# Kernel optimization log

Measured on AMD Instinct MI355X. Metric: run time of the kernel, lower is better.

Reference implementation:

```python
import jax, jax.numpy as jnp
import numpy as np

B, T_ENC, T_DEC = 1024, 96, 16
P_Q, CFG, H = 235, 32, 256
D_IN = P_Q + 5 + 10 + 3 + 3  # 256, matches input_size in __init__


def _lstm_step(x, h, c, Wih, Whh, bih, bhh):
    # torch.nn.LSTMCell: gate order i, f, g, o
    g = x @ Wih.T + bih + h @ Whh.T + bhh
    i, f, gg, o = jnp.split(g, 4, axis=-1)
    c2 = jax.nn.sigmoid(f) * c + jax.nn.sigmoid(i) * jnp.tanh(gg)
    h2 = jax.nn.sigmoid(o) * jnp.tanh(c2)
    return h2, c2


def setup_inputs():
    key = jax.random.key(0)
    ks = jax.random.split(key, 30)
    s = 0.05

    def n(i, shape):
        return jax.random.normal(ks[i], shape, jnp.float32) * s

    return {
        "input_p_q": jax.random.normal(ks[0], (B, T_ENC, P_Q), jnp.float32),
        "input_config": jax.random.normal(ks[1], (B, T_ENC, CFG), jnp.float32),
        "input_time": jax.random.randint(ks[2], (B, T_ENC, 3), 0, 5, jnp.int32),
        "W_cfg": n(3, (10, CFG)), "b_cfg": n(4, (10,)),
        "E_hour": n(5, (24, 5)), "E_wd": n(6, (8, 3)), "E_season": n(7, (5, 3)),
        "Wih_e": n(8, (4 * H, D_IN)), "Whh_e": n(9, (4 * H, H)),
        "bih_e": n(10, (4 * H,)), "bhh_e": n(11, (4 * H,)),
        "Wih_d": n(12, (4, H + 1)), "Whh_d": n(13, (4, 1)),
        "bih_d": n(14, (4,)), "bhh_d": n(15, (4,)),
        "Wi_s": n(16, (H, D_IN)), "bi_s": n(17, (H,)),
        "We_s": n(18, (H, 2 * H)),
        "Vd_s": n(19, (1, H)), "bVd_s": n(20, (1,)),
        "Wd_t": n(21, (H, H)), "bd_t": n(22, (H,)),
        "Wd2_t": n(23, (H, 2)),
        "Vd_t": n(24, (1, H)), "bVd_t": n(25, (1,)),
    }


def _forward(input_p_q, input_config, input_time, W_cfg, b_cfg, E_hour, E_wd, E_season,
             Wih_e, Whh_e, bih_e, bhh_e, Wih_d, Whh_d, bih_d, bhh_d,
             Wi_s, bi_s, We_s, Vd_s, bVd_s, Wd_t, bd_t, Wd2_t, Vd_t, bVd_t):
    b = input_p_q.shape[0]
    cfg = input_config @ W_cfg.T + b_cfg  # [B,T,10]
    inputs = jnp.concatenate([
        input_p_q, cfg,
        E_hour[input_time[:, :, 0]],
        E_wd[input_time[:, :, 1]],
        E_season[input_time[:, :, 2]],
    ], axis=2)  # [B,T,D_IN]

    # spatial_attention_Wi(inputs) hoisted out of the per-step loop (identical math)
    wi = inputs @ Wi_s.T + bi_s  # [B,T,H]

    def enc_step(carry, xt):
        hi, ci = carry
        x_t, wi_t = xt
        # Vd(tanh(We([h,c]) + Wi(x)))  -> [B,1] scalar gate (no softmax in original)
        a = jnp.tanh(jnp.concatenate([hi, ci], axis=1) @ We_s.T + wi_t) @ Vd_s.T + bVd_s
        h2, c2 = _lstm_step(x_t * a, hi, ci, Wih_e, Whh_e, bih_e, bhh_e)
        return (h2, c2), h2

    h0 = jnp.zeros((b, H), inputs.dtype)
    (_, _), mid = jax.lax.scan(enc_step, (h0, h0),
                               (inputs.transpose(1, 0, 2), wi.transpose(1, 0, 2)))
    mid = mid.transpose(1, 0, 2)  # [B,T,H]

    # temporal_attention_Wd(mid) does not depend on decode step -> hoisted
    wd_mid = mid @ Wd_t.T + bd_t  # [B,T,H]
    prev0 = mid[:, -1, 2:3]       # [B,1], as in original (element 2 of last hidden)

    def dec_step(carry, _):
        hi, ci, prev = carry
        q = jnp.concatenate([hi, ci], axis=1) @ Wd2_t.T       # [B,H]
        a = jnp.tanh(q[:, None, :] + wd_mid) @ Vd_t.T + bVd_t  # [B,T,1], raw scores
        ctx = jnp.einsum('bth,bt->bh', mid, a[..., 0])          # weighted sum over T
        h2, c2 = _lstm_step(jnp.concatenate([ctx, prev], axis=1), hi, ci,
                            Wih_d, Whh_d, bih_d, bhh_d)
        return (h2, c2, h2), h2

    z = jnp.zeros((b, 1), inputs.dtype)
    _, dec = jax.lax.scan(dec_step, (z, z, prev0), None, length=T_DEC)
    return dec.transpose(1, 0, 2)  # [B,16,1]


def reference(input_p_q, input_config, input_time, W_cfg, b_cfg, E_hour, E_wd, E_season,
              Wih_e, Whh_e, bih_e, bhh_e, Wih_d, Whh_d, bih_d, bhh_d,
              Wi_s, bi_s, We_s, Vd_s, bVd_s, Wd_t, bd_t, Wd2_t, Vd_t, bVd_t):
    return _forward(input_p_q, input_config, input_time, W_cfg, b_cfg, E_hour, E_wd,
                    E_season, Wih_e, Whh_e, bih_e, bhh_e, Wih_d, Whh_d, bih_d, bhh_d,
                    Wi_s, bi_s, We_s, Vd_s, bVd_s, Wd_t, bd_t, Wd2_t, Vd_t, bVd_t)
```

## Files before the change

kernel.cpp:

```cpp
#include <hip/hip_runtime.h>
#include <hip/hip_bf16.h>


typedef unsigned short ushort_t;
using short4v = __attribute__((ext_vector_type(4))) short;
using short8  = __attribute__((ext_vector_type(8))) short;
using floatx4 = __attribute__((ext_vector_type(4))) float;

#define DEVFN static __device__ __forceinline__

DEVFN float bs2f(ushort_t u) {
    union { float f; unsigned v; } c; c.v = ((unsigned)u) << 16; return c.f;
}
DEVFN ushort_t f2bs(float f) {
    __hip_bfloat16 h = __float2bfloat16(f);
    return *reinterpret_cast<ushort_t*>(&h);
}
DEVFN float gload(const void* p, long i, int bf) {
    if (bf) return bs2f(((const ushort_t*)p)[i]);
    return ((const float*)p)[i];
}
DEVFN float sigm(float x) { return 1.f / (1.f + __expf(-x)); }
DEVFN float ftanh(float x) {
    float t = __expf(-2.f * fabsf(x));
    float r = (1.f - t) / (1.f + t);
    return copysignf(r, x);
}
DEVFN short8 ld8(const ushort_t* p) { return *reinterpret_cast<const short8*>(p); }

DEVFN void bar_lgkm() {
    asm volatile("s_waitcnt lgkmcnt(0)" ::: "memory");
    __builtin_amdgcn_s_barrier();
}

DEVFN void gload_lds16(const ushort_t* g, ushort_t* l) {
    typedef const __attribute__((address_space(1))) unsigned int gu32;
    typedef __attribute__((address_space(3))) unsigned int lu32;
    __builtin_amdgcn_global_load_lds((gu32*)g, (lu32*)l, 16, 0, 0);
}

#define VW11() asm volatile("s_waitcnt vmcnt(11)" ::: "memory")

struct SrcPtrs { const void* p[26]; };
struct WsPtrs {
    ushort_t *wcfg, *bcfg, *eh, *ew, *es, *wis, *bis, *wes, *vds, *bvds,
             *whh, *wih, *bih, *bhh, *wdt, *bdt, *wd2t, *vdt, *bvdt,
             *wihd, *whhd, *bihd, *bhhd;
};

__global__ void k_detect(const void* probe, int* flag) {
    if (threadIdx.x == 0 && blockIdx.x == 0) {
        const ushort_t* u = (const ushort_t*)probe;
        int ok = 1;
        for (int i = 0; i < 16; ++i) {
            ushort_t v = u[2 * i];
            int e = (v >> 7) & 0xFF;
            if (!(v == 0 || (e >= 96 && e <= 126))) ok = 0;
        }
        *flag = ok;
    }
}

__global__ __launch_bounds__(256) void k_cvt(SrcPtrs sp, WsPtrs wp, const int* flagp) {
    int bf = *flagp;
    const void* src = nullptr; ushort_t* dst = nullptr; long n = 0;
    switch (blockIdx.x) {
        case 0:  src = sp.p[3];  dst = wp.wcfg; n = 320;    break;
        case 1:  src = sp.p[4];  dst = wp.bcfg; n = 10;     break;
        case 2:  src = sp.p[5];  dst = wp.eh;   n = 120;    break;
        case 3:  src = sp.p[6];  dst = wp.ew;   n = 24;     break;
        case 4:  src = sp.p[7];  dst = wp.es;   n = 15;     break;
        case 5:  src = sp.p[16]; dst = wp.wis;  n = 65536;  break;
        case 6:  src = sp.p[17]; dst = wp.bis;  n = 256;    break;
        case 8:  src = sp.p[19]; dst = wp.vds;  n = 256;    break;
        case 9:  src = sp.p[20]; dst = wp.bvds; n = 1;      break;
        case 12: src = sp.p[10]; dst = wp.bih;  n = 1024;   break;
        case 13: src = sp.p[11]; dst = wp.bhh;  n = 1024;   break;
        case 14: src = sp.p[21]; dst = wp.wdt;  n = 65536;  break;
        case 15: src = sp.p[22]; dst = wp.bdt;  n = 256;    break;
        case 16: src = sp.p[23]; dst = wp.wd2t; n = 512;    break;
        case 17: src = sp.p[24]; dst = wp.vdt;  n = 256;    break;
        case 18: src = sp.p[25]; dst = wp.bvdt; n = 1;      break;
        case 19: src = sp.p[12]; dst = wp.wihd; n = 1028;   break;
        case 20: src = sp.p[13]; dst = wp.whhd; n = 4;      break;
        case 21: src = sp.p[14]; dst = wp.bihd; n = 4;      break;
        case 22: src = sp.p[15]; dst = wp.bhhd; n = 4;      break;
        default: return;
    }
    for (long i = threadIdx.x; i < n; i += 256) {
        float v = bf ? bs2f(((const ushort_t*)src)[i]) : ((const float*)src)[i];
        dst[i] = f2bs(v);
    }
}

__global__ __launch_bounds__(256) void k_permA(
    const void* whh_src, const void* wih_src,
    ushort_t* whhp, ushort_t* wihb, const int* flagp)
{
    int bf = *flagp;
    long base = (long)blockIdx.x * 2048;
    if (blockIdx.y == 1) {
#pragma unroll
        for (int ii = 0; ii < 8; ++ii) {
            long p = base + threadIdx.x + ii * 256;
            wihb[p] = f2bs(gload(wih_src, p, bf));
        }
        return;
    }
#pragma unroll
    for (int ii = 0; ii < 8; ++ii) {
        long p = base + threadIdx.x + ii * 256;
        int c = (int)(p >> 9), l = (int)((p >> 3) & 63), e = (int)(p & 7);
        int w = c >> 5, kk = (c >> 2) & 7, g = c & 3;
        int q = l >> 4, ln = l & 15;
        long si = (long)(g * 256 + w * 16 + ln) * 256 + kk * 32 + q * 8 + e;
        whhp[p] = f2bs(gload(whh_src, si, bf));
    }
}

__global__ __launch_bounds__(256) void k_permB(
    const void* wes_src, ushort_t* wesp, const int* flagp)
{
    int bf = *flagp;
    long base = (long)blockIdx.x * 2048;
#pragma unroll
    for (int ii = 0; ii < 8; ++ii) {
        long p = base + threadIdx.x + ii * 256;
        int c = (int)(p >> 9), l = (int)((p >> 3) & 63), e = (int)(p & 7);
        int w = c >> 4, kk = c & 15;
        int q = l >> 4, ln = l & 15;
        long si = (long)(w * 16 + ln) * 512 + kk * 32 + q * 8 + e;
        wesp[p] = f2bs(gload(wes_src, si, bf));
    }
}

__global__ __launch_bounds__(256) void k_build(
    const void* __restrict__ pq, const void* __restrict__ cfg_in,
    const int* __restrict__ timei, WsPtrs wp, const int* __restrict__ flagp,
    ushort_t* __restrict__ inputs)
{
    int bf = *flagp;
    int ch = threadIdx.x;
    for (int rr = 0; rr < 4; ++rr) {
        long row = (long)blockIdx.x * 4 + rr;
        float v;
        if (ch < 235) {
            v = gload(pq, row * 235 + ch, bf);
        } else if (ch < 245) {
            int j = ch - 235;
            float acc = bs2f(wp.bcfg[j]);
            for (int k = 0; k < 32; ++k)
                acc += gload(cfg_in, row * 32 + k, bf) * bs2f(wp.wcfg[j * 32 + k]);
            v = acc;
        } else if (ch < 250) {
            v = bs2f(wp.eh[timei[row * 3 + 0] * 5 + (ch - 245)]);
        } else if (ch < 253) {
            v = bs2f(wp.ew[timei[row * 3 + 1] * 3 + (ch - 250)]);
        } else {
            v = bs2f(wp.es[timei[row * 3 + 2] * 3 + (ch - 253)]);
        }
        inputs[row * 256 + ch] = f2bs(v);
    }
}

__global__ __launch_bounds__(256) void k_gemm(
    const ushort_t* __restrict__ A, const ushort_t* __restrict__ W,
    const ushort_t* __restrict__ bias, ushort_t* __restrict__ out,
    int ostride, int gatherB)
{
    const int K = 256;
    __shared__ alignas(16) ushort_t At[128][40];
    __shared__ alignas(16) ushort_t Bt[128][40];

    int tid  = threadIdx.x;
    int lane = tid & 63, wave = tid >> 6;
    int wm = wave >> 1, wn = wave & 1;
    int q = lane >> 4, ln = lane & 15;
    long mbase = (long)blockIdx.x * 128;

    floatx4 acc[4][4];
#pragma unroll
    for (int i = 0; i < 4; ++i)
#pragma unroll
        for (int j = 0; j < 4; ++j) acc[i][j] = (floatx4){0.f, 0.f, 0.f, 0.f};

    for (int k0 = 0; k0 < K; k0 += 32) {
        __syncthreads();
#pragma unroll
        for (int it = 0; it < 2; ++it) {
            int c = tid + it * 256;
            int r = c >> 2, kc = (c & 3) * 8;
            int wrow = gatherB ? (((r & 3) << 8) + ((int)blockIdx.y << 5) + (r >> 2))
                               : ((int)blockIdx.y * 128 + r);
            *reinterpret_cast<short8*>(&At[r][kc]) = ld8(&A[(mbase + r) * K + k0 + kc]);
            *reinterpret_cast<short8*>(&Bt[r][kc]) = ld8(&W[(long)wrow * K + k0 + kc]);
        }
        __syncthreads();
        short8 af[4];
#pragma unroll
        for (int mt = 0; mt < 4; ++mt)
            af[mt] = *reinterpret_cast<const short8*>(&At[wm * 64 + mt * 16 + ln][q * 8]);
#pragma unroll
        for (int nt = 0; nt < 4; ++nt) {
            short8 bf = *reinterpret_cast<const short8*>(&Bt[wn * 64 + nt * 16 + ln][q * 8]);
#pragma unroll
            for (int mt = 0; mt < 4; ++mt)
                acc[mt][nt] = __builtin_amdgcn_mfma_f32_16x16x32_bf16(af[mt], bf, acc[mt][nt], 0, 0, 0);
        }
    }

#pragma unroll
    for (int mt = 0; mt < 4; ++mt)
#pragma unroll
        for (int nt = 0; nt < 4; ++nt)
#pragma unroll
            for (int reg = 0; reg < 4; ++reg) {
                long row = mbase + wm * 64 + mt * 16 + q * 4 + reg;
                int  col = (int)blockIdx.y * 128 + wn * 64 + nt * 16 + ln;
                float bv = bias ? bs2f(bias[col]) : 0.f;
                out[row * (long)ostride + col] = f2bs(acc[mt][nt][reg] + bv);
            }
}

#define MFMA16(a, b, c) __builtin_amdgcn_mfma_f32_16x16x32_bf16((a), (b), (c), 0, 0, 0)

DEVFN const ushort_t* sptr2(const ushort_t* const* wesW, const ushort_t* const* whhW,
                            int j) {
    int s = j & 1, c = j >> 1;
    return (c < 16) ? (wesW[s] + (c << 9)) : (whhW[s] + ((c - 16) << 9));
}

__global__ __launch_bounds__(512) void k_encoder(
    const ushort_t* __restrict__ wi, const ushort_t* __restrict__ ax,
    WsPtrs wp, ushort_t* __restrict__ mid)
{
    __shared__ ushort_t wring[8][12][512];
    __shared__ alignas(16) ushort_t hcb[2][16][520];
    __shared__ alignas(16) float aPartT[16][20];

    int tid  = threadIdx.x;
    int lane = tid & 63, w = tid >> 6;
    int q = lane >> 4, ln = lane & 15;
    long row0 = (long)blockIdx.x * 16;

    for (int i = tid; i < 2 * 16 * 520; i += 512) ((ushort_t*)hcb)[i] = 0;

    int u0 = w * 32 + ln;
    float bc[2][4], vds[2];
#pragma unroll
    for (int s = 0; s < 2; ++s) {
        int us = u0 + s * 16;
        bc[s][0] = bs2f(wp.bih[us])       + bs2f(wp.bhh[us]);
        bc[s][1] = bs2f(wp.bih[256 + us]) + bs2f(wp.bhh[256 + us]);
        bc[s][2] = bs2f(wp.bih[512 + us]) + bs2f(wp.bhh[512 + us]);
        bc[s][3] = bs2f(wp.bih[768 + us]) + bs2f(wp.bhh[768 + us]);
        vds[s]   = bs2f(wp.vds[us]);
    }
    float bVd = bs2f(wp.bvds[0]);

    const ushort_t* wesW[2]; const ushort_t* whhW[2];
#pragma unroll
    for (int s = 0; s < 2; ++s) {
        int wprime = 2 * w + s;
        wesW[s] = wp.wes + ((long)wprime << 13) + lane * 8;
        whhW[s] = wp.whh + ((long)wprime << 14) + lane * 8;
    }

    const ushort_t* wiB[4]; const ushort_t* axB[4];
#pragma unroll
    for (int reg = 0; reg < 4; ++reg) {
        long rw = (row0 + q * 4 + reg) * 96;
        wiB[reg] = wi + rw * 256 + u0;
        axB[reg] = ax + rw * 1024 + u0 * 4;
    }
    int mr = tid >> 5, mc = (tid & 31) * 8;
    ushort_t* midB = mid + (row0 + mr) * 96 * 256 + mc;

    float creg[2][4] = {{0.f, 0.f, 0.f, 0.f}, {0.f, 0.f, 0.f, 0.f}};
    __syncthreads();

#pragma unroll
    for (int j = 0; j < 12; ++j)
        gload_lds16(sptr2(wesW, whhW, j), &wring[w][j][0]);

    for (int t = 0; t < 96; ++t) {
        ushort_t (*R)[520]  = hcb[t & 1];
        ushort_t (*Wb)[520] = hcb[(t & 1) ^ 1];

        {
            long toff = (long)(t > 0 ? t - 1 : 95) * 256;
            uint4 hv = *reinterpret_cast<const uint4*>(&R[mr][mc]);
            *reinterpret_cast<uint4*>(midB + toff) = hv;
        }
        short4v axv[2][4]; float wiv[2][4];
#pragma unroll
        for (int reg = 0; reg < 4; ++reg) {
            const ushort_t* a0 = axB[reg] + (long)t * 1024;
            axv[0][reg] = *reinterpret_cast<const short4v*>(a0);
            axv[1][reg] = *reinterpret_cast<const short4v*>(a0 + 64);
            const ushort_t* w0 = wiB[reg] + (long)t * 256;
            wiv[0][reg] = bs2f(w0[0]);
            wiv[1][reg] = bs2f(w0[16]);
        }

        floatx4 acc1[2];
        acc1[0] = (floatx4){0.f, 0.f, 0.f, 0.f};
        acc1[1] = (floatx4){0.f, 0.f, 0.f, 0.f};
#pragma unroll
        for (int kk = 0; kk < 16; ++kk) {
            short8 af = ld8(&R[ln][kk * 32 + q * 8]);
#pragma unroll
            for (int s = 0; s < 2; ++s) {
                const int j = kk * 2 + s;
                VW11();
                short8 bw = ld8(&wring[w][j % 12][lane * 8]);
                acc1[s] = MFMA16(af, bw, acc1[s]);
                gload_lds16(sptr2(wesW, whhW, (j + 12) % 96), &wring[w][j % 12][0]);
            }
        }

        float p4[2][4];
#pragma unroll
        for (int s = 0; s < 2; ++s)
#pragma unroll
            for (int reg = 0; reg < 4; ++reg)
                p4[s][reg] = ftanh(acc1[s][reg] + wiv[s][reg]) * vds[s];
#pragma unroll
        for (int m = 1; m < 16; m <<= 1) {
#pragma unroll
            for (int s = 0; s < 2; ++s)
#pragma unroll
                for (int reg = 0; reg < 4; ++reg)
                    p4[s][reg] += __shfl_xor(p4[s][reg], m, 64);
        }
        if (ln == 0) {
#pragma unroll
            for (int s = 0; s < 2; ++s) {
                floatx4 pv = {p4[s][0], p4[s][1], p4[s][2], p4[s][3]};
                *reinterpret_cast<floatx4*>(&aPartT[2 * w + s][q * 4]) = pv;
            }
        }
        bar_lgkm();

        floatx4 aH[2][4];
#pragma unroll
        for (int s = 0; s < 2; ++s)
#pragma unroll
            for (int g = 0; g < 4; ++g) aH[s][g] = (floatx4){0.f, 0.f, 0.f, 0.f};
#pragma unroll
        for (int kk = 0; kk < 8; ++kk) {
            short8 af = ld8(&R[ln][kk * 32 + q * 8]);
#pragma unroll
            for (int g = 0; g < 4; ++g) {
#pragma unroll
                for (int s = 0; s < 2; ++s) {
                    const int j = 32 + (kk * 4 + g) * 2 + s;
                    VW11();
                    short8 bw = ld8(&wring[w][j % 12][lane * 8]);
                    aH[s][g] = MFMA16(af, bw, aH[s][g]);
                    gload_lds16(sptr2(wesW, whhW, (j + 12) % 96), &wring[w][j % 12][0]);
                }
            }
        }

        floatx4 av = {bVd, bVd, bVd, bVd};
#pragma unroll
        for (int ww = 0; ww < 16; ++ww)
            av += *reinterpret_cast<const floatx4*>(&aPartT[ww][q * 4]);

#pragma unroll
        for (int s = 0; s < 2; ++s) {
            int us = u0 + s * 16;
#pragma unroll
            for (int reg = 0; reg < 4; ++reg) {
                float a  = av[reg];
                float gi = aH[s][0][reg] + a * bs2f((ushort_t)axv[s][reg][0]) + bc[s][0];
                float gf = aH[s][1][reg] + a * bs2f((ushort_t)axv[s][reg][1]) + bc[s][1];
                float gg = aH[s][2][reg] + a * bs2f((ushort_t)axv[s][reg][2]) + bc[s][2];
                float go = aH[s][3][reg] + a * bs2f((ushort_t)axv[s][reg][3]) + bc[s][3];
                float c2 = sigm(gf) * creg[s][reg] + sigm(gi) * ftanh(gg);
                float h2 = sigm(go) * ftanh(c2);
                creg[s][reg] = c2;
                int r = q * 4 + reg;
                Wb[r][us] = f2bs(h2);
                Wb[r][256 + us] = f2bs(c2);
            }
        }
        bar_lgkm();
    }

    asm volatile("s_waitcnt vmcnt(0)" ::: "memory");
    {
        uint4 hv = *reinterpret_cast<const uint4*>(&hcb[0][mr][mc]);
        *reinterpret_cast<uint4*>(midB + 95L * 256) = hv;
    }
}

__global__ __launch_bounds__(256) void k_decoder(
    const ushort_t* __restrict__ mid, const ushort_t* __restrict__ wd,
    WsPtrs wp, const int* __restrict__ flagp, void* __restrict__ out)
{
    __shared__ ushort_t wdl[96][264];
    __shared__ float qL[256], aLs[96], ctxL[256], VdtL[256], gL[4];
    __shared__ float st[3];

    int tid = threadIdx.x;
    long b = blockIdx.x;
    int bf = *flagp;

    for (int c = tid; c < 96 * 256; c += 256) {
        int tp = c >> 8, chn = c & 255;
        wdl[tp][chn] = wd[(b * 96 + tp) * 256 + chn];
    }
    qL[tid] = 0.f; ctxL[tid] = 0.f;
    if (tid < 96) aLs[tid] = 0.f;
    if (tid < 4)  gL[tid] = 0.f;
    VdtL[tid] = bs2f(wp.vdt[tid]);
    if (tid == 0) {
        st[0] = 0.f; st[1] = 0.f;
        st[2] = bs2f(mid[(b * 96 + 95) * 256 + 2]);
    }
    float bVdt = bs2f(wp.bvdt[0]);
    float w2a = bs2f(wp.wd2t[tid * 2]), w2b = bs2f(wp.wd2t[tid * 2 + 1]);
    __syncthreads();

    for (int s = 0; s < 16; ++s) {
        float hi = st[0], ci = st[1], prev = st[2];
        qL[tid] = hi * w2a + ci * w2b;
        __syncthreads();
        {
            int v = tid >> 6, l = tid & 63;
            for (int tp = v; tp < 96; tp += 4) {
                float sacc = 0.f;
#pragma unroll
                for (int e = 0; e < 4; ++e) {
                    int u = l * 4 + e;
                    sacc += ftanh(qL[u] + bs2f(wdl[tp][u])) * VdtL[u];
                }
#pragma unroll
                for (int m = 1; m < 64; m <<= 1) sacc += __shfl_xor(sacc, m, 64);
                if (l == 0) aLs[tp] = sacc + bVdt;
            }
        }
        __syncthreads();
        {
            float acc = 0.f;
            for (int tp = 0; tp < 96; ++tp)
                acc += aLs[tp] * bs2f(mid[(b * 96 + tp) * 256 + tid]);
            ctxL[tid] = acc;
        }
        __syncthreads();
        {
            int g = tid >> 6, k = tid & 63;
            float part = 0.f;
#pragma unroll
            for (int e = 0; e < 4; ++e) {
                int u = k + e * 64;
                part += bs2f(wp.wihd[g * 257 + u]) * ctxL[u];
            }
#pragma unroll
            for (int m = 1; m < 64; m <<= 1) part += __shfl_xor(part, m, 64);
            if (k == 0)
                gL[g] = part + bs2f(wp.bihd[g]) + bs2f(wp.bhhd[g])
                      + bs2f(wp.whhd[g]) * hi + bs2f(wp.wihd[g * 257 + 256]) * prev;
        }
        __syncthreads();
        if (tid == 0) {
            float c2 = sigm(gL[1]) * ci + sigm(gL[0]) * ftanh(gL[2]);
            float h2 = sigm(gL[3]) * ftanh(c2);
            st[0] = h2; st[1] = c2; st[2] = h2;
            long oi = b * 16 + s;
            if (bf) ((ushort_t*)out)[oi] = f2bs(h2);
            else    ((float*)out)[oi] = h2;
        }
        __syncthreads();
    }
}

extern "C" void kernel_launch(void* const* d_in, const int* in_sizes, int n_in,
                              void* d_out, int out_size, void* d_ws, size_t ws_size,
                              hipStream_t stream)
{
    const long MT = 1024L * 96;

    int* flagp = (int*)d_ws;
    ushort_t* base = (ushort_t*)((char*)d_ws + 256);

    SrcPtrs sp;
    for (int i = 0; i < 26; ++i) sp.p[i] = d_in[i];

    static const long sizes[23] = {
        320, 10, 120, 24, 15, 65536, 256, 131072, 256, 1,
        262144, 262144, 1024, 1024, 65536, 256, 512, 256, 1,
        1028, 4, 4, 4
    };
    ushort_t* ptrs[23];
    long off = 0;
    for (int i = 0; i < 23; ++i) {
        ptrs[i] = base + off;
        off += (sizes[i] + 7) & ~7L;
    }

    WsPtrs wp;
    wp.wcfg = ptrs[0];  wp.bcfg = ptrs[1];  wp.eh   = ptrs[2];  wp.ew   = ptrs[3];
    wp.es   = ptrs[4];  wp.wis  = ptrs[5];  wp.bis  = ptrs[6];  wp.wes  = ptrs[7];
    wp.vds  = ptrs[8];  wp.bvds = ptrs[9];  wp.whh  = ptrs[10]; wp.wih  = ptrs[11];
    wp.bih  = ptrs[12]; wp.bhh  = ptrs[13]; wp.wdt  = ptrs[14]; wp.bdt  = ptrs[15];
    wp.wd2t = ptrs[16]; wp.vdt  = ptrs[17]; wp.bvdt = ptrs[18]; wp.wihd = ptrs[19];
    wp.whhd = ptrs[20]; wp.bihd = ptrs[21]; wp.bhhd = ptrs[22];

    ushort_t* inputs = base + off;
    ushort_t* wib    = inputs + MT * 256;
    ushort_t* midb   = wib + MT * 256;
    ushort_t* axb    = midb + MT * 256;
    ushort_t* wdb    = wib;

    k_detect<<<1, 64, 0, stream>>>(d_in[3], flagp);
    k_cvt<<<23, 256, 0, stream>>>(sp, wp, flagp);
    k_permA<<<dim3(128, 2), 256, 0, stream>>>(d_in[9], d_in[8], wp.whh, wp.wih, flagp);
    k_permB<<<64, 256, 0, stream>>>(d_in[18], wp.wes, flagp);
    k_build<<<24576, 256, 0, stream>>>(d_in[0], d_in[1], (const int*)d_in[2],
                                       wp, flagp, inputs);
    k_gemm<<<dim3(768, 2), 256, 0, stream>>>(inputs, wp.wis, wp.bis, wib, 256, 0);
    k_gemm<<<dim3(768, 8), 256, 0, stream>>>(inputs, wp.wih, nullptr, axb, 1024, 1);
    k_encoder<<<64, 512, 0, stream>>>(wib, axb, wp, midb);
    k_gemm<<<dim3(768, 2), 256, 0, stream>>>(midb, wp.wdt, wp.bdt, wdb, 256, 0);
    k_decoder<<<1024, 256, 0, stream>>>(midb, wdb, wp, flagp, d_out);
}
```

Before: 2.483 ms.

## Stream encoder weights directly into registers instead of an LDS ring

Drops the per-wave LDS weight ring fed by global_load_lds and instead loads each weight fragment straight into a 4-deep register ring with inline global_load_dwordx4, waiting on vmcnt(3) under a sched_barrier. The weight-stream order is reorganised so each half (s) finishes its attention and gate MFMAs in turn, and the gate MFMAs now run after the attention barrier. A large dummy shared array, touched only on an unreachable branch, pads LDS so fewer blocks share a CU. The aim is to cut LDS write/read traffic and per-step pointer arithmetic. The cost is a shallower prefetch depth that exposes more global-load latency, plus deliberately lowered occupancy.

```diff
diff --git a/kernel.cpp b/kernel.cpp
--- a/kernel.cpp
+++ b/kernel.cpp
@@ -33,13 +33,11 @@
     __builtin_amdgcn_s_barrier();
 }
 
-DEVFN void gload_lds16(const ushort_t* g, ushort_t* l) {
-    typedef const __attribute__((address_space(1))) unsigned int gu32;
-    typedef __attribute__((address_space(3))) unsigned int lu32;
-    __builtin_amdgcn_global_load_lds((gu32*)g, (lu32*)l, 16, 0, 0);
-}
-
-#define VW11() asm volatile("s_waitcnt vmcnt(11)" ::: "memory")
+#define GLD16R(dst, src) \
+    asm volatile("global_load_dwordx4 %0, %1, off" : "+v"(dst) : "v"(src))
+
+#define VW3() do { asm volatile("s_waitcnt vmcnt(3)"); \
+                   __builtin_amdgcn_sched_barrier(0x3F7); } while (0)
 
 struct SrcPtrs { const void* p[26]; };
 struct WsPtrs {
@@ -224,28 +222,22 @@
 
 #define MFMA16(a, b, c) __builtin_amdgcn_mfma_f32_16x16x32_bf16((a), (b), (c), 0, 0, 0)
 
-DEVFN const ushort_t* sptr2(const ushort_t* const* wesW, const ushort_t* const* whhW,
-                            int j) {
-    int s = j & 1, c = j >> 1;
-    return (c < 16) ? (wesW[s] + (c << 9)) : (whhW[s] + ((c - 16) << 9));
-}
-
 __global__ __launch_bounds__(512) void k_encoder(
     const ushort_t* __restrict__ wi, const ushort_t* __restrict__ ax,
     WsPtrs wp, ushort_t* __restrict__ mid)
 {
-    __shared__ ushort_t wring[8][12][512];
     __shared__ alignas(16) ushort_t hcb[2][16][520];
     __shared__ alignas(16) float aPartT[16][20];
+    __shared__ ushort_t occupancy_pad[30720];
 
     int tid  = threadIdx.x;
     int lane = tid & 63, w = tid >> 6;
     int q = lane >> 4, ln = lane & 15;
     long row0 = (long)blockIdx.x * 16;
+    int u0 = w * 32 + ln;
 
     for (int i = tid; i < 2 * 16 * 520; i += 512) ((ushort_t*)hcb)[i] = 0;
 
-    int u0 = w * 32 + ln;
     float bc[2][4], vds[2];
 #pragma unroll
     for (int s = 0; s < 2; ++s) {
@@ -258,30 +250,35 @@
     }
     float bVd = bs2f(wp.bvds[0]);
 
-    const ushort_t* wesW[2]; const ushort_t* whhW[2];
-#pragma unroll
-    for (int s = 0; s < 2; ++s) {
-        int wprime = 2 * w + s;
-        wesW[s] = wp.wes + ((long)wprime << 13) + lane * 8;
-        whhW[s] = wp.whh + ((long)wprime << 14) + lane * 8;
-    }
-
-    const ushort_t* wiB[4]; const ushort_t* axB[4];
-#pragma unroll
-    for (int reg = 0; reg < 4; ++reg) {
-        long rw = (row0 + q * 4 + reg) * 96;
-        wiB[reg] = wi + rw * 256 + u0;
-        axB[reg] = ax + rw * 1024 + u0 * 4;
-    }
+    const ushort_t* wesW0 = wp.wes + ((long)(2 * w)     << 13) + lane * 8;
+    const ushort_t* wesW1 = wp.wes + ((long)(2 * w + 1) << 13) + lane * 8;
+    const ushort_t* whhW0 = wp.whh + ((long)(2 * w)     << 14) + lane * 8;
+    const ushort_t* whhW1 = wp.whh + ((long)(2 * w + 1) << 14) + lane * 8;
+
+    const ushort_t* wiB0 = wi + ((row0 + q * 4) * 96) * 256 + u0;
+    const ushort_t* axB0 = ax + ((row0 + q * 4) * 96) * 1024 + u0 * 4;
+
     int mr = tid >> 5, mc = (tid & 31) * 8;
     ushort_t* midB = mid + (row0 + mr) * 96 * 256 + mc;
 
+    if (blockIdx.x > 60000) {
+        occupancy_pad[tid] = (ushort_t)tid;
+        midB[0] = occupancy_pad[(tid + 1) & 511];
+    }
+
     float creg[2][4] = {{0.f, 0.f, 0.f, 0.f}, {0.f, 0.f, 0.f, 0.f}};
     __syncthreads();
 
-#pragma unroll
-    for (int j = 0; j < 12; ++j)
-        gload_lds16(sptr2(wesW, whhW, j), &wring[w][j][0]);
+    auto sp3 = [&](int j) -> const ushort_t* {
+        if (j < 16)  return wesW0 + ((j & 15) << 9);
+        if (j < 32)  return wesW1 + ((j & 15) << 9);
+        if (j < 64)  return whhW0 + (((j - 32) & 31) << 9);
+        return whhW1 + (((j - 64) & 31) << 9);
+    };
+
+    short8 Wr[4] = {};
+#pragma unroll
+    for (int j = 0; j < 4; ++j) GLD16R(Wr[j], sp3(j));
 
     for (int t = 0; t < 96; ++t) {
         ushort_t (*R)[520]  = hcb[t & 1];
@@ -295,73 +292,41 @@
         short4v axv[2][4]; float wiv[2][4];
 #pragma unroll
         for (int reg = 0; reg < 4; ++reg) {
-            const ushort_t* a0 = axB[reg] + (long)t * 1024;
+            const ushort_t* a0 = axB0 + ((long)reg * 96 + t) * 1024;
             axv[0][reg] = *reinterpret_cast<const short4v*>(a0);
             axv[1][reg] = *reinterpret_cast<const short4v*>(a0 + 64);
-            const ushort_t* w0 = wiB[reg] + (long)t * 256;
+            const ushort_t* w0 = wiB0 + ((long)reg * 96 + t) * 256;
             wiv[0][reg] = bs2f(w0[0]);
             wiv[1][reg] = bs2f(w0[16]);
         }
 
-        floatx4 acc1[2];
-        acc1[0] = (floatx4){0.f, 0.f, 0.f, 0.f};
-        acc1[1] = (floatx4){0.f, 0.f, 0.f, 0.f};
-#pragma unroll
-        for (int kk = 0; kk < 16; ++kk) {
-            short8 af = ld8(&R[ln][kk * 32 + q * 8]);
-#pragma unroll
-            for (int s = 0; s < 2; ++s) {
-                const int j = kk * 2 + s;
-                VW11();
-                short8 bw = ld8(&wring[w][j % 12][lane * 8]);
-                acc1[s] = MFMA16(af, bw, acc1[s]);
-                gload_lds16(sptr2(wesW, whhW, (j + 12) % 96), &wring[w][j % 12][0]);
-            }
-        }
-
-        float p4[2][4];
-#pragma unroll
-        for (int s = 0; s < 2; ++s)
+#pragma unroll
+        for (int s = 0; s < 2; ++s) {
+            floatx4 acc1 = (floatx4){0.f, 0.f, 0.f, 0.f};
+#pragma unroll
+            for (int c = 0; c < 16; ++c) {
+                const int j = s * 16 + c;
+                short8 af = ld8(&R[ln][c * 32 + q * 8]);
+                VW3();
+                acc1 = MFMA16(af, Wr[j & 3], acc1);
+                GLD16R(Wr[j & 3], sp3((j + 4) % 96));
+            }
+            float p4[4];
 #pragma unroll
             for (int reg = 0; reg < 4; ++reg)
-                p4[s][reg] = ftanh(acc1[s][reg] + wiv[s][reg]) * vds[s];
-#pragma unroll
-        for (int m = 1; m < 16; m <<= 1) {
-#pragma unroll
-            for (int s = 0; s < 2; ++s)
+                p4[reg] = ftanh(acc1[reg] + wiv[s][reg]) * vds[s];
+#pragma unroll
+            for (int m = 1; m < 16; m <<= 1) {
 #pragma unroll
                 for (int reg = 0; reg < 4; ++reg)
-                    p4[s][reg] += __shfl_xor(p4[s][reg], m, 64);
-        }
-        if (ln == 0) {
-#pragma unroll
-            for (int s = 0; s < 2; ++s) {
-                floatx4 pv = {p4[s][0], p4[s][1], p4[s][2], p4[s][3]};
+                    p4[reg] += __shfl_xor(p4[reg], m, 64);
+            }
+            if (ln == 0) {
+                floatx4 pv = {p4[0], p4[1], p4[2], p4[3]};
                 *reinterpret_cast<floatx4*>(&aPartT[2 * w + s][q * 4]) = pv;
             }
         }
         bar_lgkm();
-
-        floatx4 aH[2][4];
-#pragma unroll
-        for (int s = 0; s < 2; ++s)
-#pragma unroll
-            for (int g = 0; g < 4; ++g) aH[s][g] = (floatx4){0.f, 0.f, 0.f, 0.f};
-#pragma unroll
-        for (int kk = 0; kk < 8; ++kk) {
-            short8 af = ld8(&R[ln][kk * 32 + q * 8]);
-#pragma unroll
-            for (int g = 0; g < 4; ++g) {
-#pragma unroll
-                for (int s = 0; s < 2; ++s) {
-                    const int j = 32 + (kk * 4 + g) * 2 + s;
-                    VW11();
-                    short8 bw = ld8(&wring[w][j % 12][lane * 8]);
-                    aH[s][g] = MFMA16(af, bw, aH[s][g]);
-                    gload_lds16(sptr2(wesW, whhW, (j + 12) % 96), &wring[w][j % 12][0]);
-                }
-            }
-        }
 
         floatx4 av = {bVd, bVd, bVd, bVd};
 #pragma unroll
@@ -370,14 +335,28 @@
 
 #pragma unroll
         for (int s = 0; s < 2; ++s) {
+            floatx4 aH[4];
+#pragma unroll
+            for (int g = 0; g < 4; ++g) aH[g] = (floatx4){0.f, 0.f, 0.f, 0.f};
+#pragma unroll
+            for (int kk = 0; kk < 8; ++kk) {
+                short8 af = ld8(&R[ln][kk * 32 + q * 8]);
+#pragma unroll
+                for (int g = 0; g < 4; ++g) {
+                    const int j = 32 + s * 32 + kk * 4 + g;
+                    VW3();
+                    aH[g] = MFMA16(af, Wr[j & 3], aH[g]);
+                    GLD16R(Wr[j & 3], sp3((j + 4) % 96));
+                }
+            }
             int us = u0 + s * 16;
 #pragma unroll
             for (int reg = 0; reg < 4; ++reg) {
                 float a  = av[reg];
-                float gi = aH[s][0][reg] + a * bs2f((ushort_t)axv[s][reg][0]) + bc[s][0];
-                float gf = aH[s][1][reg] + a * bs2f((ushort_t)axv[s][reg][1]) + bc[s][1];
-                float gg = aH[s][2][reg] + a * bs2f((ushort_t)axv[s][reg][2]) + bc[s][2];
-                float go = aH[s][3][reg] + a * bs2f((ushort_t)axv[s][reg][3]) + bc[s][3];
+                float gi = aH[0][reg] + a * bs2f((ushort_t)axv[s][reg][0]) + bc[s][0];
+                float gf = aH[1][reg] + a * bs2f((ushort_t)axv[s][reg][1]) + bc[s][1];
+                float gg = aH[2][reg] + a * bs2f((ushort_t)axv[s][reg][2]) + bc[s][2];
+                float go = aH[3][reg] + a * bs2f((ushort_t)axv[s][reg][3]) + bc[s][3];
                 float c2 = sigm(gf) * creg[s][reg] + sigm(gi) * ftanh(gg);
                 float h2 = sigm(go) * ftanh(c2);
                 creg[s][reg] = c2;
```

Result: faster. 2.287 ms (-7.9%).
